# Optimization experiments

Hardware: AMD Instinct MI355X
Metric: run time of the kernel (lower is better)

Reference implementation:

```python
import jax, jax.numpy as jnp
import numpy as np

NUM_HEADS = 16
FIELD_SIZE = 512
SIGMA = 3.0
EMB = 1024


def _causal_kernel_fft(G, sigma):
    # kernel[i] = exp(-|i - G//2| / sigma) for i < G//2, else 0; normalized
    i = np.arange(G)
    dist = np.abs(i - G // 2)
    kernel = np.where(i >= G // 2, 0.0, np.exp(-dist / sigma)).astype(np.float32)
    kernel = kernel / (kernel.sum() + 1e-8)
    return jnp.asarray(np.fft.rfft(kernel), dtype=jnp.complex64)


def setup_inputs() -> dict:
    key = jax.random.key(0)
    ks = jax.random.split(key, 9)
    B, N, D = 4, 4096, EMB
    s = 1.0 / np.sqrt(D)
    return {
        "x": jax.random.normal(ks[0], (B, N, D), dtype=jnp.float32),
        "q_w": jax.random.uniform(ks[1], (D, D), minval=-s, maxval=s, dtype=jnp.float32),
        "q_b": jnp.zeros((D,), jnp.float32),
        "k_w": jax.random.uniform(ks[2], (D, D), minval=-s, maxval=s, dtype=jnp.float32),
        "k_b": jnp.zeros((D,), jnp.float32),
        "v_w": jax.random.uniform(ks[3], (D, D), minval=-s, maxval=s, dtype=jnp.float32),
        "v_b": jnp.zeros((D,), jnp.float32),
        "out_w": jax.random.uniform(ks[4], (D, D), minval=-s, maxval=s, dtype=jnp.float32),
        "out_b": jnp.zeros((D,), jnp.float32),
    }


def reference(x, q_w, q_b, k_w, k_b, v_w, v_b, out_w, out_b):
    B, N, D = x.shape
    H, hd, G = NUM_HEADS, D // NUM_HEADS, FIELD_SIZE

    # projections (q is computed in the original but unused downstream)
    q = x @ q_w.T + q_b  # noqa: F841 (faithful to original)
    k = (x @ k_w.T + k_b).reshape(B, N, H, hd).transpose(0, 2, 1, 3)  # (B,H,N,hd)
    v = (x @ v_w.T + v_b).reshape(B, N, H, hd).transpose(0, 2, 1, 3)

    # map sequence positions -> field bins (same for all b, h)
    pos = jnp.arange(N, dtype=jnp.float32) / max(N - 1, 1) * (G - 1)
    field_idx = jnp.clip(pos.astype(jnp.int32), 0, G - 1)  # (N,)

    # weighted values by key magnitude
    k_mag = jnp.linalg.norm(k, axis=-1, keepdims=True)  # (B,H,N,1)
    wv = v * k_mag  # (B,H,N,hd)

    # scatter-add tokens into field bins (vectorized over B,H,hd)
    field = jax.ops.segment_sum(wv.transpose(2, 0, 1, 3), field_idx,
                                num_segments=G)  # (G,B,H,hd)
    field = field.transpose(1, 2, 0, 3)  # (B,H,G,hd)

    # causal convolution along the field via FFT (circular, as in original)
    kfft = _causal_kernel_fft(G, SIGMA)
    f_fft = jnp.fft.rfft(field, n=G, axis=2)
    conv = jnp.fft.irfft(f_fft * kfft[None, None, :, None], n=G, axis=2)

    # gather back to token positions
    out = conv[:, :, field_idx, :]  # (B,H,N,hd)
    out = out.transpose(0, 2, 1, 3).reshape(B, N, D)
    return out @ out_w.T + out_b
```

## Files before the change

kernel.cpp:

```cpp
#include <hip/hip_runtime.h>
#include <hip/hip_bf16.h>

#define NPOS 4096
#define DIM  1024
#define GSZ  512

#define GAS __attribute__((address_space(1)))
#define LAS __attribute__((address_space(3)))

typedef __attribute__((ext_vector_type(8))) short bf16x8;
typedef __attribute__((ext_vector_type(4))) float f32x4;

__device__ __forceinline__ void async_load16(const void* g, void* l) {
  __builtin_amdgcn_global_load_lds((const GAS void*)g, (LAS void*)l, 16, 0, 0);
}

__device__ __forceinline__ int fidx_of(int n) {
  return (int)(((float)n / 4095.0f) * 511.0f);
}

__device__ __forceinline__ float bf2f(unsigned short s) {
  union { unsigned u; float f; } v; v.u = ((unsigned)s) << 16; return v.f;
}

__device__ __forceinline__ void bin_range(int g, int& i0, int& i1) {
  i0 = (g * 4095 + 510) / 511;
  while (i0 > 0 && fidx_of(i0 - 1) >= g) --i0;
  while (i0 < NPOS && fidx_of(i0) < g) ++i0;
  if (g == GSZ - 1) { i1 = NPOS; return; }
  i1 = ((g + 1) * 4095 + 510) / 511;
  while (i1 > 0 && fidx_of(i1 - 1) >= g + 1) --i1;
  while (i1 < NPOS && fidx_of(i1) < g + 1) ++i1;
}

__global__ __launch_bounds__(256) void cast_all(
    const float* __restrict__ x, const float* __restrict__ kw,
    const float* __restrict__ vw, const float* __restrict__ ow,
    __hip_bfloat16* __restrict__ xb, __hip_bfloat16* __restrict__ kvwb,
    __hip_bfloat16* __restrict__ outwb) {
  int blk = blockIdx.x;
  const float* src; __hip_bfloat16* dst; int off;
  if (blk < 16384)      { src = x;  dst = xb;              off = blk; }
  else if (blk < 17408) { src = kw; dst = kvwb;            off = blk - 16384; }
  else if (blk < 18432) { src = vw; dst = kvwb + 1048576;  off = blk - 17408; }
  else                  { src = ow; dst = outwb;           off = blk - 18432; }
  int i = (off * 256 + threadIdx.x) * 4;
  float4 f = *(const float4*)(src + i);
  ushort4 o;
  __hip_bfloat16 t;
  t = __float2bfloat16(f.x); o.x = *(unsigned short*)&t;
  t = __float2bfloat16(f.y); o.y = *(unsigned short*)&t;
  t = __float2bfloat16(f.z); o.z = *(unsigned short*)&t;
  t = __float2bfloat16(f.w); o.w = *(unsigned short*)&t;
  *(ushort4*)(dst + i) = o;
}

__global__ __launch_bounds__(256) void gemm_kv(
    const __hip_bfloat16* __restrict__ A,
    const __hip_bfloat16* __restrict__ B,
    const float* __restrict__ k_b, const float* __restrict__ v_b,
    __hip_bfloat16* __restrict__ Vb, float* __restrict__ knorm) {
  const int K = 1024;
  __shared__ __align__(16) __hip_bfloat16 As[2][128 * 32];
  __shared__ __align__(16) __hip_bfloat16 Bs[2][128 * 32];
  const int tid = threadIdx.x;
  const int bm = blockIdx.x * 128, bn = blockIdx.y * 128;

  const int srow = tid >> 2;
  const int scol = (tid & 3) * 8;
  const __hip_bfloat16* ap0 = A + (size_t)(bm + srow) * K + scol;
  const __hip_bfloat16* ap1 = A + (size_t)(bm + srow + 64) * K + scol;
  const __hip_bfloat16* bp0 = B + (size_t)(bn + srow) * K + scol;
  const __hip_bfloat16* bp1 = B + (size_t)(bn + srow + 64) * K + scol;
  const int soff = srow * 32 + scol;

  const int wave = tid >> 6, lane = tid & 63;
  const int wm = (wave >> 1) * 64, wn = (wave & 1) * 64;
  const int m16 = lane & 15, quad = lane >> 4;

  f32x4 acc[4][4];
#pragma unroll
  for (int i = 0; i < 4; i++)
#pragma unroll
    for (int j = 0; j < 4; j++) acc[i][j] = (f32x4)0.f;

  for (int k0 = 0; k0 < K; k0 += 64) {
    async_load16(ap0 + k0, &As[0][soff]);
    async_load16(ap1 + k0, &As[0][soff + 64 * 32]);
    async_load16(bp0 + k0, &Bs[0][soff]);
    async_load16(bp1 + k0, &Bs[0][soff + 64 * 32]);
    async_load16(ap0 + k0 + 32, &As[1][soff]);
    async_load16(ap1 + k0 + 32, &As[1][soff + 64 * 32]);
    async_load16(bp0 + k0 + 32, &Bs[1][soff]);
    async_load16(bp1 + k0 + 32, &Bs[1][soff + 64 * 32]);
    __syncthreads();
#pragma unroll
    for (int h = 0; h < 2; h++) {
      bf16x8 af[4], bfr[4];
#pragma unroll
      for (int mt = 0; mt < 4; mt++)
        af[mt] = *(const bf16x8*)&As[h][(wm + mt * 16 + m16) * 32 + quad * 8];
#pragma unroll
      for (int nt = 0; nt < 4; nt++)
        bfr[nt] = *(const bf16x8*)&Bs[h][(wn + nt * 16 + m16) * 32 + quad * 8];
#pragma unroll
      for (int mt = 0; mt < 4; mt++)
#pragma unroll
        for (int nt = 0; nt < 4; nt++)
          acc[mt][nt] = __builtin_amdgcn_mfma_f32_16x16x32_bf16(af[mt], bfr[nt], acc[mt][nt], 0, 0, 0);
    }
    __syncthreads();
  }

  if (bn < 1024) {
    const int head = (bn + wn) >> 6;
    float bv[4];
#pragma unroll
    for (int nt = 0; nt < 4; nt++) bv[nt] = k_b[bn + wn + nt * 16 + m16];
#pragma unroll
    for (int mt = 0; mt < 4; mt++) {
#pragma unroll
      for (int r = 0; r < 4; r++) {
        float s = 0.f;
#pragma unroll
        for (int nt = 0; nt < 4; nt++) {
          float v = acc[mt][nt][r] + bv[nt];
          s += v * v;
        }
        s += __shfl_xor(s, 1);
        s += __shfl_xor(s, 2);
        s += __shfl_xor(s, 4);
        s += __shfl_xor(s, 8);
        if (m16 == 0) {
          int row = bm + wm + mt * 16 + quad * 4 + r;
          knorm[(size_t)row * 16 + head] = sqrtf(s);
        }
      }
    }
  } else {
#pragma unroll
    for (int mt = 0; mt < 4; mt++) {
#pragma unroll
      for (int nt = 0; nt < 4; nt++) {
        int col = bn - 1024 + wn + nt * 16 + m16;
        float bv = v_b[col];
#pragma unroll
        for (int r = 0; r < 4; r++) {
          int row = bm + wm + mt * 16 + quad * 4 + r;
          Vb[(size_t)row * 1024 + col] = __float2bfloat16(acc[mt][nt][r] + bv);
        }
      }
    }
  }
}

__global__ __launch_bounds__(256) void gemm_outc(
    const __hip_bfloat16* __restrict__ A,
    const __hip_bfloat16* __restrict__ B,
    const float* __restrict__ bias,
    float* __restrict__ C) {
  const int K = 1024;
  __shared__ __align__(16) __hip_bfloat16 As[64 * 32];
  __shared__ __align__(16) __hip_bfloat16 Bs[64 * 32];
  const int tid = threadIdx.x;
  const int bm = blockIdx.x * 64, bn = blockIdx.y * 64;

  const int srow = tid >> 2;
  const int scol = (tid & 3) * 8;
  const __hip_bfloat16* ap = A + (size_t)(bm + srow) * K + scol;
  const __hip_bfloat16* bp = B + (size_t)(bn + srow) * K + scol;
  __hip_bfloat16* as = &As[srow * 32 + scol];
  __hip_bfloat16* bs = &Bs[srow * 32 + scol];

  const int wave = tid >> 6, lane = tid & 63;
  const int wm = (wave >> 1) * 32, wn = (wave & 1) * 32;
  const int m16 = lane & 15, quad = lane >> 4;

  f32x4 acc[2][2];
#pragma unroll
  for (int i = 0; i < 2; i++)
#pragma unroll
    for (int j = 0; j < 2; j++) acc[i][j] = (f32x4)0.f;

  for (int k0 = 0; k0 < K; k0 += 32) {
    async_load16(ap + k0, as);
    async_load16(bp + k0, bs);
    __syncthreads();
    bf16x8 af[2], bfr[2];
#pragma unroll
    for (int mt = 0; mt < 2; mt++)
      af[mt] = *(const bf16x8*)&As[(wm + mt * 16 + m16) * 32 + quad * 8];
#pragma unroll
    for (int nt = 0; nt < 2; nt++)
      bfr[nt] = *(const bf16x8*)&Bs[(wn + nt * 16 + m16) * 32 + quad * 8];
#pragma unroll
    for (int mt = 0; mt < 2; mt++)
#pragma unroll
      for (int nt = 0; nt < 2; nt++)
        acc[mt][nt] = __builtin_amdgcn_mfma_f32_16x16x32_bf16(af[mt], bfr[nt], acc[mt][nt], 0, 0, 0);
    __syncthreads();
  }

#pragma unroll
  for (int mt = 0; mt < 2; mt++) {
#pragma unroll
    for (int nt = 0; nt < 2; nt++) {
      int col = bn + wn + nt * 16 + m16;
      float bv = bias[col];
#pragma unroll
      for (int r = 0; r < 4; r++) {
        int row = bm + wm + mt * 16 + quad * 4 + r;
        C[(size_t)row * 1024 + col] = acc[mt][nt][r] + bv;
      }
    }
  }
}

__global__ __launch_bounds__(256) void gather_out_kernel(
    const float* __restrict__ outc, float* __restrict__ out) {
  const int row = blockIdx.x;
  const int b = row >> 12, n = row & (NPOS - 1);
  const int g = fidx_of(n);
  const float4* src = (const float4*)(outc + ((size_t)(b * GSZ) + g) * DIM);
  float4* dst = (float4*)(out + (size_t)row * DIM);
  dst[threadIdx.x] = src[threadIdx.x];
}

__global__ __launch_bounds__(256) void wv_field_kernel(
    const __hip_bfloat16* __restrict__ V, const float* __restrict__ knorm,
    float* __restrict__ field) {
  const int b = blockIdx.x, g = blockIdx.y;
  int i0, i1;
  bin_range(g, i0, i1);
  int cnt = i1 - i0;
  if (cnt > 9) cnt = 9;
  __shared__ float km[9][16];
  const int tid = threadIdx.x;
  if (tid < 144) {
    int r = tid >> 4, h = tid & 15;
    km[r][h] = (r < cnt) ? knorm[(size_t)(b * NPOS + i0 + r) * 16 + h] : 0.f;
  }
  __syncthreads();
  const int c0 = tid * 4, h = tid >> 4;
  const unsigned short* vbase = (const unsigned short*)V + (size_t)(b * NPOS + i0) * 1024 + c0;
  ushort4 vv[8];
  float ww[8];
#pragma unroll
  for (int j = 0; j < 8; ++j) {
    int jc = (j < cnt) ? j : 0;
    vv[j] = *(const ushort4*)(vbase + (size_t)jc * 1024);
    ww[j] = (j < cnt) ? km[j][h] : 0.f;
  }
  float a0 = 0.f, a1 = 0.f, a2 = 0.f, a3 = 0.f;
#pragma unroll
  for (int j = 0; j < 8; ++j) {
    a0 += ww[j] * bf2f(vv[j].x); a1 += ww[j] * bf2f(vv[j].y);
    a2 += ww[j] * bf2f(vv[j].z); a3 += ww[j] * bf2f(vv[j].w);
  }
  if (cnt == 9) {
    ushort4 v8 = *(const ushort4*)(vbase + (size_t)8 * 1024);
    float w8 = km[8][h];
    a0 += w8 * bf2f(v8.x); a1 += w8 * bf2f(v8.y);
    a2 += w8 * bf2f(v8.z); a3 += w8 * bf2f(v8.w);
  }
  *(float4*)(field + ((size_t)(b * GSZ + g)) * DIM + c0) = make_float4(a0, a1, a2, a3);
}

__global__ __launch_bounds__(256) void conv_ema_kernel(
    const float* __restrict__ field, __hip_bfloat16* __restrict__ convb) {
  const int b = blockIdx.x, h = blockIdx.y, n0 = blockIdx.z * 64;
  __shared__ float slab[128 * 64];
  const int tid = threadIdx.x;
  const float* fb = field + (size_t)b * GSZ * DIM + h * 64;
  for (int i = tid; i < 128 * 16; i += 256) {
    int row = i >> 4, c4 = i & 15;
    int gg = (n0 + 257 + row) & (GSZ - 1);
    *(float4*)&slab[row * 64 + c4 * 4] = *(const float4*)(fb + (size_t)gg * DIM + c4 * 4);
  }
  __syncthreads();
  const float a = 0.71653131057378927f;
  const float w1 = 1.0f - a;
  const int c = tid & 63, sub = tid >> 6;
  const int e0 = sub * 16;
  float acc = 0.f;
#pragma unroll 4
  for (int t = e0 + 79; t >= e0 + 16; --t)
    acc = w1 * slab[t * 64 + c] + a * acc;
#pragma unroll
  for (int t = e0 + 15; t >= e0; --t) {
    acc = w1 * slab[t * 64 + c] + a * acc;
    convb[((size_t)(b * GSZ) + n0 + t) * DIM + h * 64 + c] = __float2bfloat16(acc);
  }
}

extern "C" void kernel_launch(void* const* d_in, const int* in_sizes, int n_in,
                              void* d_out, int out_size, void* d_ws, size_t ws_size,
                              hipStream_t stream) {
  (void)in_sizes; (void)n_in; (void)out_size; (void)ws_size;
  const float* x     = (const float*)d_in[0];
  const float* k_w   = (const float*)d_in[3];
  const float* k_b   = (const float*)d_in[4];
  const float* v_w   = (const float*)d_in[5];
  const float* v_b   = (const float*)d_in[6];
  const float* out_w = (const float*)d_in[7];
  const float* out_b = (const float*)d_in[8];

  char* p = (char*)d_ws;
  __hip_bfloat16* xb    = (__hip_bfloat16*)p;
  float*          outc  = (float*)p;          p += (size_t)16384 * 1024 * 2;
  __hip_bfloat16* kvwb  = (__hip_bfloat16*)p; p += (size_t)2048 * 1024 * 2;
  __hip_bfloat16* outwb = (__hip_bfloat16*)p; p += (size_t)1024 * 1024 * 2;
  __hip_bfloat16* Vb    = (__hip_bfloat16*)p; p += (size_t)16384 * 1024 * 2;
  float*          knorm = (float*)p;          p += (size_t)16384 * 16 * 4;
  float*          field = (float*)p;          p += (size_t)4 * 512 * 1024 * 4;
  __hip_bfloat16* convb = (__hip_bfloat16*)p;

  cast_all<<<19456, 256, 0, stream>>>(x, k_w, v_w, out_w, xb, kvwb, outwb);

  gemm_kv<<<dim3(128, 16), 256, 0, stream>>>(xb, kvwb, k_b, v_b, Vb, knorm);

  wv_field_kernel<<<dim3(4, 512), 256, 0, stream>>>(Vb, knorm, field);
  conv_ema_kernel<<<dim3(4, 16, 8), 256, 0, stream>>>(field, convb);

  gemm_outc<<<dim3(32, 16), 256, 0, stream>>>(convb, outwb, out_b, outc);
  gather_out_kernel<<<16384, 256, 0, stream>>>(outc, (float*)d_out);
}
```

Before: 266.3 us.

## Rewrite K/V projection GEMM with 256x256 tiles, swizzled LDS and pipelined staging

The K/V projection GEMM moves from 128x128 tiles with 256 threads to 256x256 tiles with 512 threads. It uses a 64-wide K stage with XOR-swizzled LDS layout and double-buffered async global-to-LDS prefetch two tiles ahead, with explicit vmcnt/lgkmcnt waits and barriers. It also adds MFMA priority hints and a remapped block order for L2 locality. The aim is higher arithmetic intensity and better overlap of loads with MFMA, at the cost of much more LDS (128KB per block) and register pressure, plus a fragile hand-written wait schedule.

```diff
diff --git a/kernel.cpp b/kernel.cpp
--- a/kernel.cpp
+++ b/kernel.cpp
@@ -55,99 +55,153 @@
   *(ushort4*)(dst + i) = o;
 }
 
-__global__ __launch_bounds__(256) void gemm_kv(
+
+#define BAR()   __builtin_amdgcn_s_barrier()
+#define LGKM0() do { asm volatile("s_waitcnt lgkmcnt(0)" ::: "memory"); \
+                     __builtin_amdgcn_sched_barrier(0); } while (0)
+#define VMW(N)  asm volatile("s_waitcnt vmcnt(" #N ")" ::: "memory")
+
+#define STAGE(BUF, KT) do { \
+    const __hip_bfloat16* ag_ = ag0 + (KT) * 64; \
+    const __hip_bfloat16* bg_ = bg0 + (KT) * 64; \
+    _Pragma("unroll") \
+    for (int c_ = 0; c_ < 4; ++c_) { \
+      async_load16(ag_ + (size_t)c_ * 65536, &As[BUF][c_ * 4096 + ldst]); \
+      async_load16(bg_ + (size_t)c_ * 65536, &Bs[BUF][c_ * 4096 + ldst]); \
+    } \
+  } while (0)
+
+#define LDA(BUF, MT, CB) (*(const bf16x8*)&As[BUF][abase + (MT) * 1024 + (CB)])
+#define LDB(BUF, NT, CB) (*(const bf16x8*)&Bs[BUF][bbase + (NT) * 1024 + (CB)])
+
+#define MFMA_Q(MQ, NQ, BF) do { \
+    __builtin_amdgcn_s_setprio(1); \
+    _Pragma("unroll") \
+    for (int m_ = 0; m_ < 4; ++m_) { \
+      _Pragma("unroll") \
+      for (int n_ = 0; n_ < 2; ++n_) { \
+        acc[(MQ)*4+m_][(NQ)*2+n_] = __builtin_amdgcn_mfma_f32_16x16x32_bf16( \
+            af[m_][0], BF[n_][0], acc[(MQ)*4+m_][(NQ)*2+n_], 0, 0, 0); \
+        acc[(MQ)*4+m_][(NQ)*2+n_] = __builtin_amdgcn_mfma_f32_16x16x32_bf16( \
+            af[m_][1], BF[n_][1], acc[(MQ)*4+m_][(NQ)*2+n_], 0, 0, 0); \
+      } \
+    } \
+    __builtin_amdgcn_s_setprio(0); \
+  } while (0)
+
+#define DO_TILE(BUF, KT) do { \
+     \
+    _Pragma("unroll") \
+    for (int m_ = 0; m_ < 4; ++m_) { af[m_][0] = LDA(BUF, m_, cb0); af[m_][1] = LDA(BUF, m_, cb1); } \
+    _Pragma("unroll") \
+    for (int n_ = 0; n_ < 2; ++n_) { b0f[n_][0] = LDB(BUF, n_, cb0); b0f[n_][1] = LDB(BUF, n_, cb1); } \
+    BAR(); LGKM0(); \
+    MFMA_Q(0, 0, b0f); \
+    BAR(); \
+     \
+    _Pragma("unroll") \
+    for (int n_ = 0; n_ < 2; ++n_) { b1f[n_][0] = LDB(BUF, 2 + n_, cb0); b1f[n_][1] = LDB(BUF, 2 + n_, cb1); } \
+    BAR(); LGKM0(); \
+    MFMA_Q(0, 1, b1f); \
+    BAR(); \
+     \
+    _Pragma("unroll") \
+    for (int m_ = 0; m_ < 4; ++m_) { af[m_][0] = LDA(BUF, 4 + m_, cb0); af[m_][1] = LDA(BUF, 4 + m_, cb1); } \
+    BAR(); LGKM0(); \
+    MFMA_Q(1, 1, b1f); \
+    BAR(); \
+     \
+    if ((KT) + 2 < 16) STAGE(BUF, (KT) + 2); \
+    BAR(); \
+    MFMA_Q(1, 0, b0f); \
+    if ((KT) + 2 < 16) { VMW(8); } else if ((KT) == 14) { VMW(0); } \
+    BAR(); \
+  } while (0)
+
+__global__ __launch_bounds__(512, 2) void gemm_kv(
     const __hip_bfloat16* __restrict__ A,
     const __hip_bfloat16* __restrict__ B,
     const float* __restrict__ k_b, const float* __restrict__ v_b,
     __hip_bfloat16* __restrict__ Vb, float* __restrict__ knorm) {
-  const int K = 1024;
-  __shared__ __align__(16) __hip_bfloat16 As[2][128 * 32];
-  __shared__ __align__(16) __hip_bfloat16 Bs[2][128 * 32];
+  __shared__ __align__(16) __hip_bfloat16 As[2][16384];
+  __shared__ __align__(16) __hip_bfloat16 Bs[2][16384];
   const int tid = threadIdx.x;
-  const int bm = blockIdx.x * 128, bn = blockIdx.y * 128;
-
-  const int srow = tid >> 2;
-  const int scol = (tid & 3) * 8;
-  const __hip_bfloat16* ap0 = A + (size_t)(bm + srow) * K + scol;
-  const __hip_bfloat16* ap1 = A + (size_t)(bm + srow + 64) * K + scol;
-  const __hip_bfloat16* bp0 = B + (size_t)(bn + srow) * K + scol;
-  const __hip_bfloat16* bp1 = B + (size_t)(bn + srow + 64) * K + scol;
-  const int soff = srow * 32 + scol;
+
+  const int l  = blockIdx.y * 64 + blockIdx.x;
+  const int vv = (l & 7) * 64 + (l >> 3);
+  const int bx = vv & 63, by = vv >> 6;
+  const int bm = bx * 256;
+
+  const int sb  = ((((tid & 7) * 16) ^ (((tid >> 3) & 7) << 4)) >> 1);
+  const int r0  = tid >> 3;
+  const __hip_bfloat16* ag0 = A + (size_t)(bm + r0) * 1024 + sb;
+  const __hip_bfloat16* bg0 = B + (size_t)(by * 256 + r0) * 1024 + sb;
+  const int ldst = tid * 8;
 
   const int wave = tid >> 6, lane = tid & 63;
-  const int wm = (wave >> 1) * 64, wn = (wave & 1) * 64;
+  const int wr = wave >> 2, wc = wave & 3;
   const int m16 = lane & 15, quad = lane >> 4;
-
-  f32x4 acc[4][4];
-#pragma unroll
-  for (int i = 0; i < 4; i++)
+  const int swz  = (m16 & 7) << 4;
+  const int cb0  = ((quad * 16)      ^ swz) >> 1;
+  const int cb1  = ((quad * 16 + 64) ^ swz) >> 1;
+  const int abase = wr * 8192 + m16 * 64;
+  const int bbase = wc * 4096 + m16 * 64;
+
+  f32x4 acc[8][4];
+#pragma unroll
+  for (int i = 0; i < 8; i++)
 #pragma unroll
     for (int j = 0; j < 4; j++) acc[i][j] = (f32x4)0.f;
 
-  for (int k0 = 0; k0 < K; k0 += 64) {
-    async_load16(ap0 + k0, &As[0][soff]);
-    async_load16(ap1 + k0, &As[0][soff + 64 * 32]);
-    async_load16(bp0 + k0, &Bs[0][soff]);
-    async_load16(bp1 + k0, &Bs[0][soff + 64 * 32]);
-    async_load16(ap0 + k0 + 32, &As[1][soff]);
-    async_load16(ap1 + k0 + 32, &As[1][soff + 64 * 32]);
-    async_load16(bp0 + k0 + 32, &Bs[1][soff]);
-    async_load16(bp1 + k0 + 32, &Bs[1][soff + 64 * 32]);
-    __syncthreads();
-#pragma unroll
-    for (int h = 0; h < 2; h++) {
-      bf16x8 af[4], bfr[4];
-#pragma unroll
-      for (int mt = 0; mt < 4; mt++)
-        af[mt] = *(const bf16x8*)&As[h][(wm + mt * 16 + m16) * 32 + quad * 8];
-#pragma unroll
-      for (int nt = 0; nt < 4; nt++)
-        bfr[nt] = *(const bf16x8*)&Bs[h][(wn + nt * 16 + m16) * 32 + quad * 8];
-#pragma unroll
-      for (int mt = 0; mt < 4; mt++)
-#pragma unroll
-        for (int nt = 0; nt < 4; nt++)
-          acc[mt][nt] = __builtin_amdgcn_mfma_f32_16x16x32_bf16(af[mt], bfr[nt], acc[mt][nt], 0, 0, 0);
-    }
-    __syncthreads();
-  }
-
-  if (bn < 1024) {
-    const int head = (bn + wn) >> 6;
+  bf16x8 af[4][2], b0f[2][2], b1f[2][2];
+
+  STAGE(0, 0);
+  STAGE(1, 1);
+  VMW(8);
+  BAR();
+
+  for (int kt = 0; kt < 16; kt += 2) {
+    DO_TILE(0, kt);
+    DO_TILE(1, kt + 1);
+  }
+
+  if (by < 4) {
+    const int head = by * 4 + wc;
     float bv[4];
 #pragma unroll
-    for (int nt = 0; nt < 4; nt++) bv[nt] = k_b[bn + wn + nt * 16 + m16];
-#pragma unroll
-    for (int mt = 0; mt < 4; mt++) {
+    for (int nt = 0; nt < 4; nt++) bv[nt] = k_b[by * 256 + wc * 64 + nt * 16 + m16];
+#pragma unroll
+    for (int mt = 0; mt < 8; mt++) {
 #pragma unroll
       for (int r = 0; r < 4; r++) {
         float s = 0.f;
 #pragma unroll
         for (int nt = 0; nt < 4; nt++) {
-          float v = acc[mt][nt][r] + bv[nt];
-          s += v * v;
+          float t = acc[mt][nt][r] + bv[nt];
+          s += t * t;
         }
         s += __shfl_xor(s, 1);
         s += __shfl_xor(s, 2);
         s += __shfl_xor(s, 4);
         s += __shfl_xor(s, 8);
         if (m16 == 0) {
-          int row = bm + wm + mt * 16 + quad * 4 + r;
+          int row = bm + wr * 128 + mt * 16 + quad * 4 + r;
           knorm[(size_t)row * 16 + head] = sqrtf(s);
         }
       }
     }
   } else {
-#pragma unroll
-    for (int mt = 0; mt < 4; mt++) {
+    const int colb = (by - 4) * 256 + wc * 64;
+#pragma unroll
+    for (int mt = 0; mt < 8; mt++) {
 #pragma unroll
       for (int nt = 0; nt < 4; nt++) {
-        int col = bn - 1024 + wn + nt * 16 + m16;
-        float bv = v_b[col];
+        int col = colb + nt * 16 + m16;
+        float bvv = v_b[col];
 #pragma unroll
         for (int r = 0; r < 4; r++) {
-          int row = bm + wm + mt * 16 + quad * 4 + r;
-          Vb[(size_t)row * 1024 + col] = __float2bfloat16(acc[mt][nt][r] + bv);
+          int row = bm + wr * 128 + mt * 16 + quad * 4 + r;
+          Vb[(size_t)row * 1024 + col] = __float2bfloat16(acc[mt][nt][r] + bvv);
         }
       }
     }
@@ -160,8 +214,8 @@
     const float* __restrict__ bias,
     float* __restrict__ C) {
   const int K = 1024;
-  __shared__ __align__(16) __hip_bfloat16 As[64 * 32];
-  __shared__ __align__(16) __hip_bfloat16 Bs[64 * 32];
+  __shared__ __align__(16) __hip_bfloat16 Aso[64 * 32];
+  __shared__ __align__(16) __hip_bfloat16 Bso[64 * 32];
   const int tid = threadIdx.x;
   const int bm = blockIdx.x * 64, bn = blockIdx.y * 64;
 
@@ -169,8 +223,8 @@
   const int scol = (tid & 3) * 8;
   const __hip_bfloat16* ap = A + (size_t)(bm + srow) * K + scol;
   const __hip_bfloat16* bp = B + (size_t)(bn + srow) * K + scol;
-  __hip_bfloat16* as = &As[srow * 32 + scol];
-  __hip_bfloat16* bs = &Bs[srow * 32 + scol];
+  __hip_bfloat16* as = &Aso[srow * 32 + scol];
+  __hip_bfloat16* bs = &Bso[srow * 32 + scol];
 
   const int wave = tid >> 6, lane = tid & 63;
   const int wm = (wave >> 1) * 32, wn = (wave & 1) * 32;
@@ -186,18 +240,18 @@
     async_load16(ap + k0, as);
     async_load16(bp + k0, bs);
     __syncthreads();
-    bf16x8 af[2], bfr[2];
+    bf16x8 afr[2], bfr[2];
 #pragma unroll
     for (int mt = 0; mt < 2; mt++)
-      af[mt] = *(const bf16x8*)&As[(wm + mt * 16 + m16) * 32 + quad * 8];
+      afr[mt] = *(const bf16x8*)&Aso[(wm + mt * 16 + m16) * 32 + quad * 8];
 #pragma unroll
     for (int nt = 0; nt < 2; nt++)
-      bfr[nt] = *(const bf16x8*)&Bs[(wn + nt * 16 + m16) * 32 + quad * 8];
+      bfr[nt] = *(const bf16x8*)&Bso[(wn + nt * 16 + m16) * 32 + quad * 8];
 #pragma unroll
     for (int mt = 0; mt < 2; mt++)
 #pragma unroll
       for (int nt = 0; nt < 2; nt++)
-        acc[mt][nt] = __builtin_amdgcn_mfma_f32_16x16x32_bf16(af[mt], bfr[nt], acc[mt][nt], 0, 0, 0);
+        acc[mt][nt] = __builtin_amdgcn_mfma_f32_16x16x32_bf16(afr[mt], bfr[nt], acc[mt][nt], 0, 0, 0);
     __syncthreads();
   }
 
@@ -317,7 +371,7 @@
 
   cast_all<<<19456, 256, 0, stream>>>(x, k_w, v_w, out_w, xb, kvwb, outwb);
 
-  gemm_kv<<<dim3(128, 16), 256, 0, stream>>>(xb, kvwb, k_b, v_b, Vb, knorm);
+  gemm_kv<<<dim3(64, 8), 512, 0, stream>>>(xb, kvwb, k_b, v_b, Vb, knorm);
 
   wv_field_kernel<<<dim3(4, 512), 256, 0, stream>>>(Vb, knorm, field);
   conv_ema_kernel<<<dim3(4, 16, 8), 256, 0, stream>>>(field, convb);
```

Measured after the change: 264.1 us. No clear change (-0.8%).
